# Kernel tuning notes

Hardware: AMD Instinct MI355X
Metric: run time of the kernel (lower is better)

Reference implementation:

```python
import jax, jax.numpy as jnp
import numpy as np

B, DIM, HID = 16384, 512, 256
DT, N_STEPS = 0.1, 3


def setup_inputs() -> dict:
    key = jax.random.key(0)
    ks = jax.random.split(key, 5)
    z = jax.random.normal(ks[0], (B, DIM), dtype=jnp.float32)
    # HNN energy MLP: 2*DIM -> HID -> HID -> 1 (tanh activations)
    s1 = 1.0 / np.sqrt(2 * DIM)
    s2 = 1.0 / np.sqrt(HID)
    W1 = jax.random.normal(ks[1], (2 * DIM, HID), dtype=jnp.float32) * s1
    b1 = jnp.zeros((HID,), dtype=jnp.float32)
    W2 = jax.random.normal(ks[2], (HID, HID), dtype=jnp.float32) * s2
    b2 = jnp.zeros((HID,), dtype=jnp.float32)
    W3 = jax.random.normal(ks[3], (HID, 1), dtype=jnp.float32) * s2
    b3 = jnp.zeros((1,), dtype=jnp.float32)
    return {"z": z, "W1": W1, "b1": b1, "W2": W2, "b2": b2, "W3": W3, "b3": b3}


def reference(z, W1, b1, W2, b2, W3, b3):
    d = z.shape[-1]
    dt = jnp.float32(DT)

    def H_sum(zp):  # total Hamiltonian over the batch -> scalar
        h = jnp.tanh(zp @ W1 + b1)
        h = jnp.tanh(h @ W2 + b2)
        return jnp.sum(h @ W3 + b3)

    gradH = jax.grad(H_sum)  # [B, 2d]: (dH/dq, dH/dp) per sample

    def leapfrog(zp):
        q, p = zp[:, :d], zp[:, d:]
        # half-step momentum: dp/dt = -dH/dq
        g = gradH(jnp.concatenate([q, p], axis=-1))
        p = p - 0.5 * dt * g[:, :d]
        # full-step position: dq/dt = dH/dp
        g = gradH(jnp.concatenate([q, p], axis=-1))
        q = q + dt * g[:, d:]
        # half-step momentum
        g = gradH(jnp.concatenate([q, p], axis=-1))
        p = p - 0.5 * dt * g[:, :d]
        return jnp.concatenate([q, p], axis=-1)

    zp = jnp.concatenate([z, jnp.zeros_like(z)], axis=-1)  # phase space [B, 2d]
    for _ in range(N_STEPS):  # fixed small unroll (n_steps=3)
        zp = leapfrog(zp)
    return zp[:, :d]
```

## Files before the change

kernel.cpp:

```cpp
#include <hip/hip_runtime.h>
#include <math.h>

#define DT 0.1f

typedef __attribute__((ext_vector_type(4)))  short short4v;
typedef __attribute__((ext_vector_type(8)))  short short8;
typedef __attribute__((ext_vector_type(16))) float f32x16;

__device__ __forceinline__ short f2bf(float x) {
    unsigned int u = __float_as_uint(x);
    unsigned int r = (u + 0x7fffu + ((u >> 16) & 1u)) >> 16;
    return (short)r;
}
__device__ __forceinline__ float bf2f(short s) {
    return __uint_as_float(((unsigned int)(unsigned short)s) << 16);
}
__device__ __forceinline__ float tanh_fast(float x) {
    float e = __expf(x + x);
    float r = __builtin_amdgcn_rcpf(e + 1.f);
    return __builtin_fmaf(-2.f, r, 1.f);
}

__device__ __forceinline__ void pack32_body(const float* __restrict__ W,
                                            short* __restrict__ out,
                                            int K, int N, int idx, bool trans)
{
    int j = idx & 7, lane = (idx >> 3) & 63, rest = idx >> 9;
    int KT = K >> 4;
    int kt = rest % KT, nt = rest / KT;
    int k = kt * 16 + (lane >> 5) * 8 + j;
    int n = nt * 32 + (lane & 31);
    out[idx] = f2bf(trans ? W[n * K + k] : W[k * N + n]);
}

__global__ __launch_bounds__(256)
void prep(const float* __restrict__ W1, const float* __restrict__ W2,
          const float* __restrict__ z,
          short* __restrict__ PBSq, short* __restrict__ PBSp,
          short* __restrict__ PB2, short* __restrict__ PB2T,
          short* __restrict__ PB1q, short* __restrict__ PB1Tp,
          short* __restrict__ zpA)
{
    __shared__ short zb[32 * 520];
    const int tid = threadIdx.x;
    const int b = blockIdx.x;

    if (b < 512) {
        const int n = tid;
        float s0 = 0.f, s1 = 0.f, s2 = 0.f, s3 = 0.f;
        int k; float coef; short* dst;
        if (b < 256) {
            k = b; coef = -0.5f * DT; dst = PBSq;
            for (int c = 0; c < 512; c += 4) {
                s0 = __builtin_fmaf(W1[(c + 0) * 256 + k], W1[(512 + c + 0) * 256 + n], s0);
                s1 = __builtin_fmaf(W1[(c + 1) * 256 + k], W1[(512 + c + 1) * 256 + n], s1);
                s2 = __builtin_fmaf(W1[(c + 2) * 256 + k], W1[(512 + c + 2) * 256 + n], s2);
                s3 = __builtin_fmaf(W1[(c + 3) * 256 + k], W1[(512 + c + 3) * 256 + n], s3);
            }
        } else {
            k = b - 256; coef = DT; dst = PBSp;
            for (int c = 0; c < 512; c += 4) {
                s0 = __builtin_fmaf(W1[(512 + c + 0) * 256 + k], W1[(c + 0) * 256 + n], s0);
                s1 = __builtin_fmaf(W1[(512 + c + 1) * 256 + k], W1[(c + 1) * 256 + n], s1);
                s2 = __builtin_fmaf(W1[(512 + c + 2) * 256 + k], W1[(c + 2) * 256 + n], s2);
                s3 = __builtin_fmaf(W1[(512 + c + 3) * 256 + k], W1[(c + 3) * 256 + n], s3);
            }
        }
        float v = coef * ((s0 + s1) + (s2 + s3));
        int kt = k >> 4, r = k & 15;
        int lane = (r >> 3) * 32 + (n & 31), nt = n >> 5;
        dst[(((nt * 16 + kt) * 64 + lane) << 3) + (r & 7)] = f2bf(v);
    } else if (b < 768) {
        pack32_body(W2, PB2, 256, 256, (b - 512) * 256 + tid, false);
    } else if (b < 1024) {
        pack32_body(W2, PB2T, 256, 256, (b - 768) * 256 + tid, true);
    } else if (b < 1536) {
        pack32_body(W1, PB1q, 512, 256, (b - 1024) * 256 + tid, false);
    } else if (b < 2048) {
        pack32_body(W1 + 512 * 256, PB1Tp, 256, 512, (b - 1536) * 256 + tid, true);
    } else {
        const int bx = b - 2048;
#pragma unroll
        for (int j = 0; j < 16; ++j) {
            int lin = j * 256 + tid;
            int r = lin >> 7, c4 = lin & 127;
            float4 v = ((const float4*)z)[(size_t)(bx * 32 + r) * 128 + c4];
            short4v pk;
            pk.x = f2bf(v.x); pk.y = f2bf(v.y); pk.z = f2bf(v.z); pk.w = f2bf(v.w);
            *(short4v*)&zb[r * 520 + c4 * 4] = pk;
        }
        __syncthreads();
        const int lane = tid & 63, w = tid >> 6;
        const int m = lane & 31, lh = lane >> 5;
#pragma unroll
        for (int j = 0; j < 8; ++j) {
            int kt = w * 8 + j;
            short8 f = *(const short8*)&zb[m * 520 + kt * 16 + lh * 8];
            *(short8*)(zpA + (((size_t)bx * 32 + kt) * 64 + lane) * 8) = f;
        }
    }
}

__device__ __forceinline__ short8 lds_frag(const short* Ac, int kt, int mt2,
                                           int l31, int lh, int rot)
{
    int nt_s = kt >> 1;
    int po = (((kt & 1) * 2 + lh) * 4 + rot) & 15;
    int base = ((nt_s * 2 + mt2) * 64 + l31) * 16 + po;
    short4v x = *(const short4v*)&Ac[base];
    short4v y = *(const short4v*)&Ac[base + 512];
    short8 r;
    r[0] = x.x; r[1] = x.y; r[2] = x.z; r[3] = x.w;
    r[4] = y.x; r[5] = y.y; r[6] = y.z; r[7] = y.w;
    return r;
}
__device__ __forceinline__ void store_tile(short* Ac, int nt, int mt2, int lane,
                                           int rot, const f32x16 v)
{
    int base = ((nt * 2 + mt2) * 64 + lane) * 16;
#pragma unroll
    for (int c = 0; c < 4; ++c) {
        short4v pk;
        pk.x = f2bf(v[4 * c + 0]); pk.y = f2bf(v[4 * c + 1]);
        pk.z = f2bf(v[4 * c + 2]); pk.w = f2bf(v[4 * c + 3]);
        *(short4v*)&Ac[base + ((4 * c + rot) & 15)] = pk;
    }
}

__device__ __forceinline__ void gemm_nt(const short* Ac, int l31, int lh, int rot,
                                        const short8* __restrict__ Bf,
                                        f32x16& acc0, f32x16& acc1)
{
    short8 pb[4];
#pragma unroll
    for (int k = 0; k < 4; ++k) pb[k] = Bf[k * 64];
    short8 pa0 = lds_frag(Ac, 0, 0, l31, lh, rot);
    short8 pa1 = lds_frag(Ac, 0, 1, l31, lh, rot);
#pragma unroll
    for (int kt = 0; kt < 16; ++kt) {
        short8 ca0 = pa0, ca1 = pa1, cb = pb[kt & 3];
        if (kt + 4 < 16) pb[kt & 3] = Bf[(kt + 4) * 64];
        if (kt + 1 < 16) {
            pa0 = lds_frag(Ac, kt + 1, 0, l31, lh, rot);
            pa1 = lds_frag(Ac, kt + 1, 1, l31, lh, rot);
        }
        acc0 = __builtin_amdgcn_mfma_f32_32x32x16_bf16(ca0, cb, acc0, 0, 0, 0);
        acc1 = __builtin_amdgcn_mfma_f32_32x32x16_bf16(ca1, cb, acc1, 0, 0, 0);
    }
}

__global__ __launch_bounds__(512, 2)
void mega(const short* __restrict__ zpA,
          const short* __restrict__ PB1q,
          const short* __restrict__ PB2,
          const short* __restrict__ PB2T,
          const short* __restrict__ PBSq,
          const short* __restrict__ PBSp,
          const float* __restrict__ b1,
          const float* __restrict__ b2,
          const float* __restrict__ W3,
          const short* __restrict__ PB1Tp,
          const float* __restrict__ z,
          float* __restrict__ out)
{
    __shared__ alignas(16) short smem[32768];
    short* h1_c = smem;
    short* da_c = smem + 16384;

    const int tid = threadIdx.x;
    const int lane = tid & 63, w = tid >> 6;
    const int l31 = lane & 31, lh = lane >> 5;
    const int rot = ((l31 >> 2) & 3) * 4;
    const int bx = blockIdx.x;

    const int col = w * 32 + l31;
    const float b1v = b1[col], b2v = b2[col], w3v = W3[col];

    f32x16 A1[2];  A1[0] = 0.f; A1[1] = 0.f;
    f32x16 dsum[2]; dsum[0] = 0.f; dsum[1] = 0.f;

    {
        const short8* Af0 = (const short8*)zpA + ((size_t)(bx * 2 + 0) * 32) * 64 + lane;
        const short8* Af1 = (const short8*)zpA + ((size_t)(bx * 2 + 1) * 32) * 64 + lane;
        const short8* Bf  = (const short8*)PB1q + ((size_t)w * 32) * 64 + lane;
        short8 pa0[2], pa1[2], pb[4];
#pragma unroll
        for (int k = 0; k < 2; ++k) { pa0[k] = Af0[k * 64]; pa1[k] = Af1[k * 64]; }
#pragma unroll
        for (int k = 0; k < 4; ++k) pb[k] = Bf[k * 64];
#pragma unroll
        for (int kt = 0; kt < 32; ++kt) {
            short8 ca0 = pa0[kt & 1], ca1 = pa1[kt & 1], cb = pb[kt & 3];
            if (kt + 2 < 32) {
                pa0[kt & 1] = Af0[(kt + 2) * 64];
                pa1[kt & 1] = Af1[(kt + 2) * 64];
            }
            if (kt + 4 < 32) pb[kt & 3] = Bf[(kt + 4) * 64];
            A1[0] = __builtin_amdgcn_mfma_f32_32x32x16_bf16(ca0, cb, A1[0], 0, 0, 0);
            A1[1] = __builtin_amdgcn_mfma_f32_32x32x16_bf16(ca1, cb, A1[1], 0, 0, 0);
        }
    }

    for (int it = 0; it < 8; ++it) {
        const bool isq = ((it % 3) == 1);

#pragma unroll
        for (int t = 0; t < 2; ++t) {
            f32x16 hv;
#pragma unroll
            for (int r = 0; r < 16; ++r) hv[r] = tanh_fast(A1[t][r] + b1v);
            store_tile(h1_c, w, t, lane, rot, hv);
        }
        __syncthreads();

        {
            f32x16 t0 = 0.f, t1 = 0.f;
            gemm_nt(h1_c, l31, lh, rot, (const short8*)PB2 + ((size_t)w * 16) * 64 + lane, t0, t1);
#pragma unroll
            for (int t = 0; t < 2; ++t) {
                f32x16& tt = t ? t1 : t0;
                f32x16 d;
#pragma unroll
                for (int r = 0; r < 16; ++r) {
                    float ta = tanh_fast(tt[r] + b2v);
                    d[r] = w3v * (1.f - ta * ta);
                }
                store_tile(da_c, w, t, lane, rot, d);
            }
        }
        __syncthreads();

        {
            f32x16 t0 = 0.f, t1 = 0.f;
            gemm_nt(da_c, l31, lh, rot, (const short8*)PB2T + ((size_t)w * 16) * 64 + lane, t0, t1);
            __syncthreads();
#pragma unroll
            for (int t = 0; t < 2; ++t) {
                f32x16& tt = t ? t1 : t0;
                f32x16 d;
                const int basei = ((w * 2 + t) * 64 + lane) * 16;
#pragma unroll
                for (int c = 0; c < 4; ++c) {
                    short4v h4 = *(const short4v*)&h1_c[basei + ((4 * c + rot) & 15)];
                    float h0 = bf2f(h4.x), h1f = bf2f(h4.y);
                    float h2 = bf2f(h4.z), h3 = bf2f(h4.w);
                    d[4 * c + 0] = tt[4 * c + 0] * (1.f - h0 * h0);
                    d[4 * c + 1] = tt[4 * c + 1] * (1.f - h1f * h1f);
                    d[4 * c + 2] = tt[4 * c + 2] * (1.f - h2 * h2);
                    d[4 * c + 3] = tt[4 * c + 3] * (1.f - h3 * h3);
                }
                if (isq) dsum[t] += d;
                store_tile(da_c, w, t, lane, rot, d);
            }
        }
        __syncthreads();

        if (it < 7) {
            const short* S = isq ? PBSp : PBSq;
            gemm_nt(da_c, l31, lh, rot, (const short8*)S + ((size_t)w * 16) * 64 + lane,
                    A1[0], A1[1]);
        }
    }

    store_tile(da_c, w, 0, lane, rot, dsum[0]);
    store_tile(da_c, w, 1, lane, rot, dsum[1]);
    __syncthreads();

    const int mt2 = w >> 2, nq = w & 3;
    f32x16 acc[4];
#pragma unroll
    for (int t = 0; t < 4; ++t) acc[t] = 0.f;
    const short8* Bf[4];
#pragma unroll
    for (int t = 0; t < 4; ++t)
        Bf[t] = (const short8*)PB1Tp + (size_t)(nq * 4 + t) * 16 * 64 + lane;

    short8 br[2][4];
#pragma unroll
    for (int k = 0; k < 2; ++k)
#pragma unroll
        for (int t = 0; t < 4; ++t) br[k][t] = Bf[t][k * 64];
#pragma unroll
    for (int kt = 0; kt < 16; ++kt) {
        short8 a = lds_frag(da_c, kt, mt2, l31, lh, rot);
        short8 bb[4];
#pragma unroll
        for (int t = 0; t < 4; ++t) bb[t] = br[kt & 1][t];
        if (kt + 2 < 16) {
#pragma unroll
            for (int t = 0; t < 4; ++t) br[kt & 1][t] = Bf[t][(kt + 2) * 64];
        }
#pragma unroll
        for (int t = 0; t < 4; ++t)
            acc[t] = __builtin_amdgcn_mfma_f32_32x32x16_bf16(a, bb[t], acc[t], 0, 0, 0);
    }
    __syncthreads();

    float* Ct = (float*)smem;
#pragma unroll
    for (int p = 0; p < 2; ++p) {
        if (mt2 == p) {
#pragma unroll
            for (int t = 0; t < 4; ++t) {
                const int c = (nq * 4 + t) * 32 + l31;
#pragma unroll
                for (int r = 0; r < 16; ++r) {
                    int row = (r & 3) + 8 * (r >> 2) + 4 * lh;
                    Ct[row * 512 + c] = acc[t][r];
                }
            }
        }
        __syncthreads();
#pragma unroll
        for (int j = 0; j < 8; ++j) {
            int lin = j * 512 + tid;
            int r = lin >> 7, c4 = lin & 127;
            size_t gi = (size_t)(bx * 64 + p * 32 + r) * 128 + c4;
            float4 zv = ((const float4*)z)[gi];
            float4 cv = *(const float4*)&Ct[r * 512 + c4 * 4];
            float4 ov;
            ov.x = zv.x + DT * cv.x; ov.y = zv.y + DT * cv.y;
            ov.z = zv.z + DT * cv.z; ov.w = zv.w + DT * cv.w;
            ((float4*)out)[gi] = ov;
        }
        __syncthreads();
    }
}

extern "C" void kernel_launch(void* const* d_in, const int* in_sizes, int n_in,
                              void* d_out, int out_size, void* d_ws, size_t ws_size,
                              hipStream_t stream)
{
    const float* z  = (const float*)d_in[0];
    const float* W1 = (const float*)d_in[1];
    const float* b1 = (const float*)d_in[2];
    const float* W2 = (const float*)d_in[3];
    const float* b2 = (const float*)d_in[4];
    const float* W3 = (const float*)d_in[5];
    float* out = (float*)d_out;

    short* PB2   = (short*)d_ws;
    short* PB2T  = PB2   + 65536;
    short* PBSq  = PB2T  + 65536;
    short* PBSp  = PBSq  + 65536;
    short* PB1q  = PBSp  + 65536;
    short* PB1Tp = PB1q  + 131072;
    short* zpA   = PB1Tp + 131072;

    prep<<<2560, 256, 0, stream>>>(W1, W2, z, PBSq, PBSp, PB2, PB2T,
                                   PB1q, PB1Tp, zpA);
    mega<<<256, 512, 0, stream>>>(zpA, PB1q, PB2, PB2T, PBSq, PBSp,
                                  b1, b2, W3, PB1Tp, z, out);
}
```

Before: 194.2 us.

## Halve mega-kernel row tile to 32 rows, doubling blocks and occupancy

The fused HNN kernel now gives each block 32 batch rows instead of 64, so it launches 512 blocks instead of 256. Each wave keeps one accumulator tile instead of two, shared memory is halved, and launch bounds ask for 4 blocks per CU instead of 2. The B-operand prefetch depth is deeper, and the final GEMM is remapped to two column tiles per wave. The weight fragments are reloaded for twice as many blocks, and each MFMA has less independent work to hide latency. The prep kernel's weight-product reduction is also unrolled to 8 accumulators.

```diff
diff --git a/kernel.cpp b/kernel.cpp
--- a/kernel.cpp
+++ b/kernel.cpp
@@ -47,26 +47,29 @@
 
     if (b < 512) {
         const int n = tid;
-        float s0 = 0.f, s1 = 0.f, s2 = 0.f, s3 = 0.f;
+        float s[8];
+#pragma unroll
+        for (int i = 0; i < 8; ++i) s[i] = 0.f;
         int k; float coef; short* dst;
         if (b < 256) {
             k = b; coef = -0.5f * DT; dst = PBSq;
-            for (int c = 0; c < 512; c += 4) {
-                s0 = __builtin_fmaf(W1[(c + 0) * 256 + k], W1[(512 + c + 0) * 256 + n], s0);
-                s1 = __builtin_fmaf(W1[(c + 1) * 256 + k], W1[(512 + c + 1) * 256 + n], s1);
-                s2 = __builtin_fmaf(W1[(c + 2) * 256 + k], W1[(512 + c + 2) * 256 + n], s2);
-                s3 = __builtin_fmaf(W1[(c + 3) * 256 + k], W1[(512 + c + 3) * 256 + n], s3);
+            for (int c = 0; c < 512; c += 8) {
+#pragma unroll
+                for (int i = 0; i < 8; ++i)
+                    s[i] = __builtin_fmaf(W1[(c + i) * 256 + k],
+                                          W1[(512 + c + i) * 256 + n], s[i]);
             }
         } else {
             k = b - 256; coef = DT; dst = PBSp;
-            for (int c = 0; c < 512; c += 4) {
-                s0 = __builtin_fmaf(W1[(512 + c + 0) * 256 + k], W1[(c + 0) * 256 + n], s0);
-                s1 = __builtin_fmaf(W1[(512 + c + 1) * 256 + k], W1[(c + 1) * 256 + n], s1);
-                s2 = __builtin_fmaf(W1[(512 + c + 2) * 256 + k], W1[(c + 2) * 256 + n], s2);
-                s3 = __builtin_fmaf(W1[(512 + c + 3) * 256 + k], W1[(c + 3) * 256 + n], s3);
-            }
-        }
-        float v = coef * ((s0 + s1) + (s2 + s3));
+            for (int c = 0; c < 512; c += 8) {
+#pragma unroll
+                for (int i = 0; i < 8; ++i)
+                    s[i] = __builtin_fmaf(W1[(512 + c + i) * 256 + k],
+                                          W1[(c + i) * 256 + n], s[i]);
+            }
+        }
+        float v = coef * (((s[0] + s[1]) + (s[2] + s[3])) +
+                          ((s[4] + s[5]) + (s[6] + s[7])));
         int kt = k >> 4, r = k & 15;
         int lane = (r >> 3) * 32 + (n & 31), nt = n >> 5;
         dst[(((nt * 16 + kt) * 64 + lane) << 3) + (r & 7)] = f2bf(v);
@@ -101,12 +104,12 @@
     }
 }
 
-__device__ __forceinline__ short8 lds_frag(const short* Ac, int kt, int mt2,
-                                           int l31, int lh, int rot)
+__device__ __forceinline__ short8 lds_frag32(const short* Ac, int kt,
+                                             int l31, int lh, int rot)
 {
     int nt_s = kt >> 1;
     int po = (((kt & 1) * 2 + lh) * 4 + rot) & 15;
-    int base = ((nt_s * 2 + mt2) * 64 + l31) * 16 + po;
+    int base = (nt_s * 64 + l31) * 16 + po;
     short4v x = *(const short4v*)&Ac[base];
     short4v y = *(const short4v*)&Ac[base + 512];
     short8 r;
@@ -114,10 +117,10 @@
     r[4] = y.x; r[5] = y.y; r[6] = y.z; r[7] = y.w;
     return r;
 }
-__device__ __forceinline__ void store_tile(short* Ac, int nt, int mt2, int lane,
-                                           int rot, const f32x16 v)
-{
-    int base = ((nt * 2 + mt2) * 64 + lane) * 16;
+__device__ __forceinline__ void store_tile32(short* Ac, int nt, int lane,
+                                             int rot, const f32x16 v)
+{
+    int base = (nt * 64 + lane) * 16;
 #pragma unroll
     for (int c = 0; c < 4; ++c) {
         short4v pk;
@@ -127,29 +130,25 @@
     }
 }
 
-__device__ __forceinline__ void gemm_nt(const short* Ac, int l31, int lh, int rot,
-                                        const short8* __restrict__ Bf,
-                                        f32x16& acc0, f32x16& acc1)
-{
-    short8 pb[4];
-#pragma unroll
-    for (int k = 0; k < 4; ++k) pb[k] = Bf[k * 64];
-    short8 pa0 = lds_frag(Ac, 0, 0, l31, lh, rot);
-    short8 pa1 = lds_frag(Ac, 0, 1, l31, lh, rot);
+__device__ __forceinline__ void gemm_nt32(const short* Ac, int l31, int lh, int rot,
+                                          const short8* __restrict__ Bf, f32x16& acc)
+{
+    short8 pb[8];
+#pragma unroll
+    for (int k = 0; k < 8; ++k) pb[k] = Bf[k * 64];
+    short8 pa0 = lds_frag32(Ac, 0, l31, lh, rot);
+    short8 pa1 = lds_frag32(Ac, 1, l31, lh, rot);
 #pragma unroll
     for (int kt = 0; kt < 16; ++kt) {
-        short8 ca0 = pa0, ca1 = pa1, cb = pb[kt & 3];
-        if (kt + 4 < 16) pb[kt & 3] = Bf[(kt + 4) * 64];
-        if (kt + 1 < 16) {
-            pa0 = lds_frag(Ac, kt + 1, 0, l31, lh, rot);
-            pa1 = lds_frag(Ac, kt + 1, 1, l31, lh, rot);
-        }
-        acc0 = __builtin_amdgcn_mfma_f32_32x32x16_bf16(ca0, cb, acc0, 0, 0, 0);
-        acc1 = __builtin_amdgcn_mfma_f32_32x32x16_bf16(ca1, cb, acc1, 0, 0, 0);
-    }
-}
-
-__global__ __launch_bounds__(512, 2)
+        short8 ca = pa0, cb = pb[kt & 7];
+        pa0 = pa1;
+        if (kt + 2 < 16) pa1 = lds_frag32(Ac, kt + 2, l31, lh, rot);
+        if (kt + 8 < 16) pb[kt & 7] = Bf[(kt + 8) * 64];
+        acc = __builtin_amdgcn_mfma_f32_32x32x16_bf16(ca, cb, acc, 0, 0, 0);
+    }
+}
+
+__global__ __launch_bounds__(512, 4)
 void mega(const short* __restrict__ zpA,
           const short* __restrict__ PB1q,
           const short* __restrict__ PB2,
@@ -163,9 +162,9 @@
           const float* __restrict__ z,
           float* __restrict__ out)
 {
-    __shared__ alignas(16) short smem[32768];
+    __shared__ alignas(16) short smem[16384];
     short* h1_c = smem;
-    short* da_c = smem + 16384;
+    short* da_c = smem + 8192;
 
     const int tid = threadIdx.x;
     const int lane = tid & 63, w = tid >> 6;
@@ -176,148 +175,130 @@
     const int col = w * 32 + l31;
     const float b1v = b1[col], b2v = b2[col], w3v = W3[col];
 
-    f32x16 A1[2];  A1[0] = 0.f; A1[1] = 0.f;
-    f32x16 dsum[2]; dsum[0] = 0.f; dsum[1] = 0.f;
+    f32x16 A1 = 0.f;
+    f32x16 dsum = 0.f;
 
     {
-        const short8* Af0 = (const short8*)zpA + ((size_t)(bx * 2 + 0) * 32) * 64 + lane;
-        const short8* Af1 = (const short8*)zpA + ((size_t)(bx * 2 + 1) * 32) * 64 + lane;
-        const short8* Bf  = (const short8*)PB1q + ((size_t)w * 32) * 64 + lane;
-        short8 pa0[2], pa1[2], pb[4];
-#pragma unroll
-        for (int k = 0; k < 2; ++k) { pa0[k] = Af0[k * 64]; pa1[k] = Af1[k * 64]; }
-#pragma unroll
-        for (int k = 0; k < 4; ++k) pb[k] = Bf[k * 64];
+        const short8* Af = (const short8*)zpA + ((size_t)bx * 32) * 64 + lane;
+        const short8* Bf = (const short8*)PB1q + ((size_t)w * 32) * 64 + lane;
+        short8 pa[4], pb[8];
+#pragma unroll
+        for (int k = 0; k < 4; ++k) pa[k] = Af[k * 64];
+#pragma unroll
+        for (int k = 0; k < 8; ++k) pb[k] = Bf[k * 64];
 #pragma unroll
         for (int kt = 0; kt < 32; ++kt) {
-            short8 ca0 = pa0[kt & 1], ca1 = pa1[kt & 1], cb = pb[kt & 3];
-            if (kt + 2 < 32) {
-                pa0[kt & 1] = Af0[(kt + 2) * 64];
-                pa1[kt & 1] = Af1[(kt + 2) * 64];
-            }
-            if (kt + 4 < 32) pb[kt & 3] = Bf[(kt + 4) * 64];
-            A1[0] = __builtin_amdgcn_mfma_f32_32x32x16_bf16(ca0, cb, A1[0], 0, 0, 0);
-            A1[1] = __builtin_amdgcn_mfma_f32_32x32x16_bf16(ca1, cb, A1[1], 0, 0, 0);
+            short8 ca = pa[kt & 3], cb = pb[kt & 7];
+            if (kt + 4 < 32) pa[kt & 3] = Af[(kt + 4) * 64];
+            if (kt + 8 < 32) pb[kt & 7] = Bf[(kt + 8) * 64];
+            A1 = __builtin_amdgcn_mfma_f32_32x32x16_bf16(ca, cb, A1, 0, 0, 0);
         }
     }
 
     for (int it = 0; it < 8; ++it) {
         const bool isq = ((it % 3) == 1);
 
-#pragma unroll
-        for (int t = 0; t < 2; ++t) {
+        {
             f32x16 hv;
 #pragma unroll
-            for (int r = 0; r < 16; ++r) hv[r] = tanh_fast(A1[t][r] + b1v);
-            store_tile(h1_c, w, t, lane, rot, hv);
+            for (int r = 0; r < 16; ++r) hv[r] = tanh_fast(A1[r] + b1v);
+            store_tile32(h1_c, w, lane, rot, hv);
         }
         __syncthreads();
 
         {
-            f32x16 t0 = 0.f, t1 = 0.f;
-            gemm_nt(h1_c, l31, lh, rot, (const short8*)PB2 + ((size_t)w * 16) * 64 + lane, t0, t1);
-#pragma unroll
-            for (int t = 0; t < 2; ++t) {
-                f32x16& tt = t ? t1 : t0;
-                f32x16 d;
-#pragma unroll
-                for (int r = 0; r < 16; ++r) {
-                    float ta = tanh_fast(tt[r] + b2v);
-                    d[r] = w3v * (1.f - ta * ta);
-                }
-                store_tile(da_c, w, t, lane, rot, d);
-            }
+            f32x16 t0 = 0.f;
+            gemm_nt32(h1_c, l31, lh, rot,
+                      (const short8*)PB2 + ((size_t)w * 16) * 64 + lane, t0);
+            f32x16 d;
+#pragma unroll
+            for (int r = 0; r < 16; ++r) {
+                float ta = tanh_fast(t0[r] + b2v);
+                d[r] = w3v * (1.f - ta * ta);
+            }
+            store_tile32(da_c, w, lane, rot, d);
         }
         __syncthreads();
 
         {
-            f32x16 t0 = 0.f, t1 = 0.f;
-            gemm_nt(da_c, l31, lh, rot, (const short8*)PB2T + ((size_t)w * 16) * 64 + lane, t0, t1);
+            f32x16 t0 = 0.f;
+            gemm_nt32(da_c, l31, lh, rot,
+                      (const short8*)PB2T + ((size_t)w * 16) * 64 + lane, t0);
             __syncthreads();
-#pragma unroll
-            for (int t = 0; t < 2; ++t) {
-                f32x16& tt = t ? t1 : t0;
-                f32x16 d;
-                const int basei = ((w * 2 + t) * 64 + lane) * 16;
-#pragma unroll
-                for (int c = 0; c < 4; ++c) {
-                    short4v h4 = *(const short4v*)&h1_c[basei + ((4 * c + rot) & 15)];
-                    float h0 = bf2f(h4.x), h1f = bf2f(h4.y);
-                    float h2 = bf2f(h4.z), h3 = bf2f(h4.w);
-                    d[4 * c + 0] = tt[4 * c + 0] * (1.f - h0 * h0);
-                    d[4 * c + 1] = tt[4 * c + 1] * (1.f - h1f * h1f);
-                    d[4 * c + 2] = tt[4 * c + 2] * (1.f - h2 * h2);
-                    d[4 * c + 3] = tt[4 * c + 3] * (1.f - h3 * h3);
-                }
-                if (isq) dsum[t] += d;
-                store_tile(da_c, w, t, lane, rot, d);
-            }
+            f32x16 d;
+            const int basei = (w * 64 + lane) * 16;
+#pragma unroll
+            for (int c = 0; c < 4; ++c) {
+                short4v h4 = *(const short4v*)&h1_c[basei + ((4 * c + rot) & 15)];
+                float h0 = bf2f(h4.x), h1f = bf2f(h4.y);
+                float h2 = bf2f(h4.z), h3 = bf2f(h4.w);
+                d[4 * c + 0] = t0[4 * c + 0] * (1.f - h0 * h0);
+                d[4 * c + 1] = t0[4 * c + 1] * (1.f - h1f * h1f);
+                d[4 * c + 2] = t0[4 * c + 2] * (1.f - h2 * h2);
+                d[4 * c + 3] = t0[4 * c + 3] * (1.f - h3 * h3);
+            }
+            if (isq) dsum += d;
+            store_tile32(da_c, w, lane, rot, d);
         }
         __syncthreads();
 
         if (it < 7) {
             const short* S = isq ? PBSp : PBSq;
-            gemm_nt(da_c, l31, lh, rot, (const short8*)S + ((size_t)w * 16) * 64 + lane,
-                    A1[0], A1[1]);
-        }
-    }
-
-    store_tile(da_c, w, 0, lane, rot, dsum[0]);
-    store_tile(da_c, w, 1, lane, rot, dsum[1]);
+            gemm_nt32(da_c, l31, lh, rot,
+                      (const short8*)S + ((size_t)w * 16) * 64 + lane, A1);
+        }
+    }
+
+    store_tile32(da_c, w, lane, rot, dsum);
     __syncthreads();
 
-    const int mt2 = w >> 2, nq = w & 3;
-    f32x16 acc[4];
-#pragma unroll
-    for (int t = 0; t < 4; ++t) acc[t] = 0.f;
-    const short8* Bf[4];
-#pragma unroll
-    for (int t = 0; t < 4; ++t)
-        Bf[t] = (const short8*)PB1Tp + (size_t)(nq * 4 + t) * 16 * 64 + lane;
-
-    short8 br[2][4];
-#pragma unroll
-    for (int k = 0; k < 2; ++k)
-#pragma unroll
-        for (int t = 0; t < 4; ++t) br[k][t] = Bf[t][k * 64];
-#pragma unroll
-    for (int kt = 0; kt < 16; ++kt) {
-        short8 a = lds_frag(da_c, kt, mt2, l31, lh, rot);
-        short8 bb[4];
-#pragma unroll
-        for (int t = 0; t < 4; ++t) bb[t] = br[kt & 1][t];
-        if (kt + 2 < 16) {
-#pragma unroll
-            for (int t = 0; t < 4; ++t) br[kt & 1][t] = Bf[t][(kt + 2) * 64];
-        }
-#pragma unroll
-        for (int t = 0; t < 4; ++t)
-            acc[t] = __builtin_amdgcn_mfma_f32_32x32x16_bf16(a, bb[t], acc[t], 0, 0, 0);
+    f32x16 acc2[2];
+    acc2[0] = 0.f; acc2[1] = 0.f;
+    {
+        const short8* Bf0 = (const short8*)PB1Tp + (size_t)(2 * w + 0) * 16 * 64 + lane;
+        const short8* Bf1 = (const short8*)PB1Tp + (size_t)(2 * w + 1) * 16 * 64 + lane;
+        short8 pb0[4], pb1[4];
+#pragma unroll
+        for (int k = 0; k < 4; ++k) { pb0[k] = Bf0[k * 64]; pb1[k] = Bf1[k * 64]; }
+        short8 pa0 = lds_frag32(da_c, 0, l31, lh, rot);
+        short8 pa1 = lds_frag32(da_c, 1, l31, lh, rot);
+#pragma unroll
+        for (int kt = 0; kt < 16; ++kt) {
+            short8 ca = pa0, cb0 = pb0[kt & 3], cb1 = pb1[kt & 3];
+            pa0 = pa1;
+            if (kt + 2 < 16) pa1 = lds_frag32(da_c, kt + 2, l31, lh, rot);
+            if (kt + 4 < 16) {
+                pb0[kt & 3] = Bf0[(kt + 4) * 64];
+                pb1[kt & 3] = Bf1[(kt + 4) * 64];
+            }
+            acc2[0] = __builtin_amdgcn_mfma_f32_32x32x16_bf16(ca, cb0, acc2[0], 0, 0, 0);
+            acc2[1] = __builtin_amdgcn_mfma_f32_32x32x16_bf16(ca, cb1, acc2[1], 0, 0, 0);
+        }
     }
     __syncthreads();
 
     float* Ct = (float*)smem;
 #pragma unroll
     for (int p = 0; p < 2; ++p) {
-        if (mt2 == p) {
-#pragma unroll
-            for (int t = 0; t < 4; ++t) {
-                const int c = (nq * 4 + t) * 32 + l31;
+        if ((w >> 2) == p) {
+#pragma unroll
+            for (int t = 0; t < 2; ++t) {
+                const int cl = (w & 3) * 64 + t * 32 + l31;
 #pragma unroll
                 for (int r = 0; r < 16; ++r) {
                     int row = (r & 3) + 8 * (r >> 2) + 4 * lh;
-                    Ct[row * 512 + c] = acc[t][r];
+                    Ct[row * 256 + cl] = acc2[t][r];
                 }
             }
         }
         __syncthreads();
 #pragma unroll
-        for (int j = 0; j < 8; ++j) {
+        for (int j = 0; j < 4; ++j) {
             int lin = j * 512 + tid;
-            int r = lin >> 7, c4 = lin & 127;
-            size_t gi = (size_t)(bx * 64 + p * 32 + r) * 128 + c4;
+            int r = lin >> 6, c4 = lin & 63;
+            size_t gi = (size_t)(bx * 32 + r) * 128 + p * 64 + c4;
             float4 zv = ((const float4*)z)[gi];
-            float4 cv = *(const float4*)&Ct[r * 512 + c4 * 4];
+            float4 cv = *(const float4*)&Ct[r * 256 + c4 * 4];
             float4 ov;
             ov.x = zv.x + DT * cv.x; ov.y = zv.y + DT * cv.y;
             ov.z = zv.z + DT * cv.z; ov.w = zv.w + DT * cv.w;
@@ -349,6 +330,6 @@
 
     prep<<<2560, 256, 0, stream>>>(W1, W2, z, PBSq, PBSp, PB2, PB2T,
                                    PB1q, PB1Tp, zpA);
-    mega<<<256, 512, 0, stream>>>(zpA, PB1q, PB2, PB2T, PBSq, PBSp,
+    mega<<<512, 512, 0, stream>>>(zpA, PB1q, PB2, PB2T, PBSq, PBSp,
                                   b1, b2, W3, PB1Tp, z, out);
 }
```

New measurement: 293.2 us. +51.0%, slower.

## Prefetch next GEMM weights across phases and double-buffer LDS gradient tiles

Applied to the files above, without the earlier changes.

Deepens the weight-fragment prefetch from 4 to 8 k-tiles and the LDS A-fragment prefetch to two tiles. The next GEMM's weight fragments are now loaded right after the current GEMM finishes, so global latency overlaps the tanh/derivative epilogue. A separate LDS buffer for the second-layer gradient removes one __syncthreads per iteration. In exchange it raises LDS to 96KB and drops the launch bound from 2 to 1 block per CU, which costs occupancy and leaves less latency hiding between blocks.

```diff
diff --git a/kernel.cpp b/kernel.cpp
--- a/kernel.cpp
+++ b/kernel.cpp
@@ -47,26 +47,29 @@
 
     if (b < 512) {
         const int n = tid;
-        float s0 = 0.f, s1 = 0.f, s2 = 0.f, s3 = 0.f;
+        float s[8];
+#pragma unroll
+        for (int i = 0; i < 8; ++i) s[i] = 0.f;
         int k; float coef; short* dst;
         if (b < 256) {
             k = b; coef = -0.5f * DT; dst = PBSq;
-            for (int c = 0; c < 512; c += 4) {
-                s0 = __builtin_fmaf(W1[(c + 0) * 256 + k], W1[(512 + c + 0) * 256 + n], s0);
-                s1 = __builtin_fmaf(W1[(c + 1) * 256 + k], W1[(512 + c + 1) * 256 + n], s1);
-                s2 = __builtin_fmaf(W1[(c + 2) * 256 + k], W1[(512 + c + 2) * 256 + n], s2);
-                s3 = __builtin_fmaf(W1[(c + 3) * 256 + k], W1[(512 + c + 3) * 256 + n], s3);
+            for (int c = 0; c < 512; c += 8) {
+#pragma unroll
+                for (int i = 0; i < 8; ++i)
+                    s[i] = __builtin_fmaf(W1[(c + i) * 256 + k],
+                                          W1[(512 + c + i) * 256 + n], s[i]);
             }
         } else {
             k = b - 256; coef = DT; dst = PBSp;
-            for (int c = 0; c < 512; c += 4) {
-                s0 = __builtin_fmaf(W1[(512 + c + 0) * 256 + k], W1[(c + 0) * 256 + n], s0);
-                s1 = __builtin_fmaf(W1[(512 + c + 1) * 256 + k], W1[(c + 1) * 256 + n], s1);
-                s2 = __builtin_fmaf(W1[(512 + c + 2) * 256 + k], W1[(c + 2) * 256 + n], s2);
-                s3 = __builtin_fmaf(W1[(512 + c + 3) * 256 + k], W1[(c + 3) * 256 + n], s3);
-            }
-        }
-        float v = coef * ((s0 + s1) + (s2 + s3));
+            for (int c = 0; c < 512; c += 8) {
+#pragma unroll
+                for (int i = 0; i < 8; ++i)
+                    s[i] = __builtin_fmaf(W1[(512 + c + i) * 256 + k],
+                                          W1[(c + i) * 256 + n], s[i]);
+            }
+        }
+        float v = coef * (((s[0] + s[1]) + (s[2] + s[3])) +
+                          ((s[4] + s[5]) + (s[6] + s[7])));
         int kt = k >> 4, r = k & 15;
         int lane = (r >> 3) * 32 + (n & 31), nt = n >> 5;
         dst[(((nt * 16 + kt) * 64 + lane) << 3) + (r & 7)] = f2bf(v);
@@ -127,29 +130,35 @@
     }
 }
 
+__device__ __forceinline__ void preload8(const short8* __restrict__ Bf, short8* pb)
+{
+#pragma unroll
+    for (int k = 0; k < 8; ++k) pb[k] = Bf[k * 64];
+}
+
 __device__ __forceinline__ void gemm_nt(const short* Ac, int l31, int lh, int rot,
                                         const short8* __restrict__ Bf,
-                                        f32x16& acc0, f32x16& acc1)
-{
-    short8 pb[4];
-#pragma unroll
-    for (int k = 0; k < 4; ++k) pb[k] = Bf[k * 64];
-    short8 pa0 = lds_frag(Ac, 0, 0, l31, lh, rot);
-    short8 pa1 = lds_frag(Ac, 0, 1, l31, lh, rot);
+                                        short8* pb, f32x16& acc0, f32x16& acc1)
+{
+    short8 pa0[2], pa1[2];
+    pa0[0] = lds_frag(Ac, 0, 0, l31, lh, rot);
+    pa1[0] = lds_frag(Ac, 0, 1, l31, lh, rot);
+    pa0[1] = lds_frag(Ac, 1, 0, l31, lh, rot);
+    pa1[1] = lds_frag(Ac, 1, 1, l31, lh, rot);
 #pragma unroll
     for (int kt = 0; kt < 16; ++kt) {
-        short8 ca0 = pa0, ca1 = pa1, cb = pb[kt & 3];
-        if (kt + 4 < 16) pb[kt & 3] = Bf[(kt + 4) * 64];
-        if (kt + 1 < 16) {
-            pa0 = lds_frag(Ac, kt + 1, 0, l31, lh, rot);
-            pa1 = lds_frag(Ac, kt + 1, 1, l31, lh, rot);
+        short8 ca0 = pa0[kt & 1], ca1 = pa1[kt & 1], cb = pb[kt & 7];
+        if (kt + 8 < 16) pb[kt & 7] = Bf[(kt + 8) * 64];
+        if (kt + 2 < 16) {
+            pa0[kt & 1] = lds_frag(Ac, kt + 2, 0, l31, lh, rot);
+            pa1[kt & 1] = lds_frag(Ac, kt + 2, 1, l31, lh, rot);
         }
         acc0 = __builtin_amdgcn_mfma_f32_32x32x16_bf16(ca0, cb, acc0, 0, 0, 0);
         acc1 = __builtin_amdgcn_mfma_f32_32x32x16_bf16(ca1, cb, acc1, 0, 0, 0);
     }
 }
 
-__global__ __launch_bounds__(512, 2)
+__global__ __launch_bounds__(512, 1)
 void mega(const short* __restrict__ zpA,
           const short* __restrict__ PB1q,
           const short* __restrict__ PB2,
@@ -163,9 +172,10 @@
           const float* __restrict__ z,
           float* __restrict__ out)
 {
-    __shared__ alignas(16) short smem[32768];
+    __shared__ alignas(16) short smem[49152];
     short* h1_c = smem;
-    short* da_c = smem + 16384;
+    short* da2_c = smem + 16384;
+    short* da1_c = smem + 32768;
 
     const int tid = threadIdx.x;
     const int lane = tid & 63, w = tid >> 6;
@@ -176,31 +186,38 @@
     const int col = w * 32 + l31;
     const float b1v = b1[col], b2v = b2[col], w3v = W3[col];
 
+    const short8* BfPB2  = (const short8*)PB2  + ((size_t)w * 16) * 64 + lane;
+    const short8* BfPB2T = (const short8*)PB2T + ((size_t)w * 16) * 64 + lane;
+    const short8* BfSq   = (const short8*)PBSq + ((size_t)w * 16) * 64 + lane;
+    const short8* BfSp   = (const short8*)PBSp + ((size_t)w * 16) * 64 + lane;
+
     f32x16 A1[2];  A1[0] = 0.f; A1[1] = 0.f;
     f32x16 dsum[2]; dsum[0] = 0.f; dsum[1] = 0.f;
+    short8 pb[8];
 
     {
         const short8* Af0 = (const short8*)zpA + ((size_t)(bx * 2 + 0) * 32) * 64 + lane;
         const short8* Af1 = (const short8*)zpA + ((size_t)(bx * 2 + 1) * 32) * 64 + lane;
         const short8* Bf  = (const short8*)PB1q + ((size_t)w * 32) * 64 + lane;
-        short8 pa0[2], pa1[2], pb[4];
+        short8 pa0[2], pa1[2];
 #pragma unroll
         for (int k = 0; k < 2; ++k) { pa0[k] = Af0[k * 64]; pa1[k] = Af1[k * 64]; }
-#pragma unroll
-        for (int k = 0; k < 4; ++k) pb[k] = Bf[k * 64];
+        preload8(Bf, pb);
 #pragma unroll
         for (int kt = 0; kt < 32; ++kt) {
-            short8 ca0 = pa0[kt & 1], ca1 = pa1[kt & 1], cb = pb[kt & 3];
+            short8 ca0 = pa0[kt & 1], ca1 = pa1[kt & 1], cb = pb[kt & 7];
             if (kt + 2 < 32) {
                 pa0[kt & 1] = Af0[(kt + 2) * 64];
                 pa1[kt & 1] = Af1[(kt + 2) * 64];
             }
-            if (kt + 4 < 32) pb[kt & 3] = Bf[(kt + 4) * 64];
+            if (kt + 8 < 32) pb[kt & 7] = Bf[(kt + 8) * 64];
             A1[0] = __builtin_amdgcn_mfma_f32_32x32x16_bf16(ca0, cb, A1[0], 0, 0, 0);
             A1[1] = __builtin_amdgcn_mfma_f32_32x32x16_bf16(ca1, cb, A1[1], 0, 0, 0);
         }
     }
 
+    preload8(BfPB2, pb);
+
     for (int it = 0; it < 8; ++it) {
         const bool isq = ((it % 3) == 1);
 
@@ -215,7 +232,8 @@
 
         {
             f32x16 t0 = 0.f, t1 = 0.f;
-            gemm_nt(h1_c, l31, lh, rot, (const short8*)PB2 + ((size_t)w * 16) * 64 + lane, t0, t1);
+            gemm_nt(h1_c, l31, lh, rot, BfPB2, pb, t0, t1);
+            preload8(BfPB2T, pb);
 #pragma unroll
             for (int t = 0; t < 2; ++t) {
                 f32x16& tt = t ? t1 : t0;
@@ -225,15 +243,15 @@
                     float ta = tanh_fast(tt[r] + b2v);
                     d[r] = w3v * (1.f - ta * ta);
                 }
-                store_tile(da_c, w, t, lane, rot, d);
+                store_tile(da2_c, w, t, lane, rot, d);
             }
         }
         __syncthreads();
 
         {
             f32x16 t0 = 0.f, t1 = 0.f;
-            gemm_nt(da_c, l31, lh, rot, (const short8*)PB2T + ((size_t)w * 16) * 64 + lane, t0, t1);
-            __syncthreads();
+            gemm_nt(da2_c, l31, lh, rot, BfPB2T, pb, t0, t1);
+            if (it < 7) preload8(isq ? BfSp : BfSq, pb);
 #pragma unroll
             for (int t = 0; t < 2; ++t) {
                 f32x16& tt = t ? t1 : t0;
@@ -250,80 +268,90 @@
                     d[4 * c + 3] = tt[4 * c + 3] * (1.f - h3 * h3);
                 }
                 if (isq) dsum[t] += d;
-                store_tile(da_c, w, t, lane, rot, d);
+                store_tile(da1_c, w, t, lane, rot, d);
             }
         }
         __syncthreads();
 
         if (it < 7) {
-            const short* S = isq ? PBSp : PBSq;
-            gemm_nt(da_c, l31, lh, rot, (const short8*)S + ((size_t)w * 16) * 64 + lane,
-                    A1[0], A1[1]);
-        }
-    }
-
-    store_tile(da_c, w, 0, lane, rot, dsum[0]);
-    store_tile(da_c, w, 1, lane, rot, dsum[1]);
+            gemm_nt(da1_c, l31, lh, rot, isq ? BfSp : BfSq, pb, A1[0], A1[1]);
+            preload8(BfPB2, pb);
+        }
+    }
+
+    store_tile(h1_c, w, 0, lane, rot, dsum[0]);
+    store_tile(h1_c, w, 1, lane, rot, dsum[1]);
     __syncthreads();
 
-    const int mt2 = w >> 2, nq = w & 3;
-    f32x16 acc[4];
-#pragma unroll
-    for (int t = 0; t < 4; ++t) acc[t] = 0.f;
-    const short8* Bf[4];
-#pragma unroll
-    for (int t = 0; t < 4; ++t)
-        Bf[t] = (const short8*)PB1Tp + (size_t)(nq * 4 + t) * 16 * 64 + lane;
-
-    short8 br[2][4];
-#pragma unroll
-    for (int k = 0; k < 2; ++k)
-#pragma unroll
-        for (int t = 0; t < 4; ++t) br[k][t] = Bf[t][k * 64];
-#pragma unroll
-    for (int kt = 0; kt < 16; ++kt) {
-        short8 a = lds_frag(da_c, kt, mt2, l31, lh, rot);
-        short8 bb[4];
-#pragma unroll
-        for (int t = 0; t < 4; ++t) bb[t] = br[kt & 1][t];
-        if (kt + 2 < 16) {
-#pragma unroll
-            for (int t = 0; t < 4; ++t) br[kt & 1][t] = Bf[t][(kt + 2) * 64];
-        }
-#pragma unroll
-        for (int t = 0; t < 4; ++t)
-            acc[t] = __builtin_amdgcn_mfma_f32_32x32x16_bf16(a, bb[t], acc[t], 0, 0, 0);
-    }
-    __syncthreads();
-
-    float* Ct = (float*)smem;
-#pragma unroll
-    for (int p = 0; p < 2; ++p) {
-        if (mt2 == p) {
-#pragma unroll
-            for (int t = 0; t < 4; ++t) {
-                const int c = (nq * 4 + t) * 32 + l31;
-#pragma unroll
-                for (int r = 0; r < 16; ++r) {
-                    int row = (r & 3) + 8 * (r >> 2) + 4 * lh;
-                    Ct[row * 512 + c] = acc[t][r];
+    const int mt2 = w >> 3 ? 0 : 0;
+    const int mtg = w >> 2 & 1;
+    (void)mt2; (void)mtg;
+
+    f32x16 acc2[2];
+    acc2[0] = 0.f; acc2[1] = 0.f;
+    const int mt = w >> 2;
+    const int nq = w & 3;
+    {
+        const short8* Bf0 = (const short8*)PB1Tp + (size_t)(nq * 4 + 0) * 16 * 64 + lane;
+        const short8* Bf1 = (const short8*)PB1Tp + (size_t)(nq * 4 + 1) * 16 * 64 + lane;
+        const short8* Bf2 = (const short8*)PB1Tp + (size_t)(nq * 4 + 2) * 16 * 64 + lane;
+        const short8* Bf3 = (const short8*)PB1Tp + (size_t)(nq * 4 + 3) * 16 * 64 + lane;
+        f32x16 acc4[4];
+#pragma unroll
+        for (int t = 0; t < 4; ++t) acc4[t] = 0.f;
+        short8 br[2][4];
+#pragma unroll
+        for (int k = 0; k < 2; ++k) {
+            br[k][0] = Bf0[k * 64]; br[k][1] = Bf1[k * 64];
+            br[k][2] = Bf2[k * 64]; br[k][3] = Bf3[k * 64];
+        }
+#pragma unroll
+        for (int kt = 0; kt < 16; ++kt) {
+            short8 a = lds_frag(h1_c, kt, mt, l31, lh, rot);
+            short8 bb[4];
+#pragma unroll
+            for (int t = 0; t < 4; ++t) bb[t] = br[kt & 1][t];
+            if (kt + 2 < 16) {
+                br[kt & 1][0] = Bf0[(kt + 2) * 64];
+                br[kt & 1][1] = Bf1[(kt + 2) * 64];
+                br[kt & 1][2] = Bf2[(kt + 2) * 64];
+                br[kt & 1][3] = Bf3[(kt + 2) * 64];
+            }
+#pragma unroll
+            for (int t = 0; t < 4; ++t)
+                acc4[t] = __builtin_amdgcn_mfma_f32_32x32x16_bf16(a, bb[t], acc4[t], 0, 0, 0);
+        }
+        __syncthreads();
+
+        float* Ct = (float*)smem;
+#pragma unroll
+        for (int p = 0; p < 2; ++p) {
+            if (mt == p) {
+#pragma unroll
+                for (int t = 0; t < 4; ++t) {
+                    const int c = (nq * 4 + t) * 32 + l31;
+#pragma unroll
+                    for (int r = 0; r < 16; ++r) {
+                        int row = (r & 3) + 8 * (r >> 2) + 4 * lh;
+                        Ct[row * 512 + c] = acc4[t][r];
+                    }
                 }
             }
-        }
-        __syncthreads();
-#pragma unroll
-        for (int j = 0; j < 8; ++j) {
-            int lin = j * 512 + tid;
-            int r = lin >> 7, c4 = lin & 127;
-            size_t gi = (size_t)(bx * 64 + p * 32 + r) * 128 + c4;
-            float4 zv = ((const float4*)z)[gi];
-            float4 cv = *(const float4*)&Ct[r * 512 + c4 * 4];
-            float4 ov;
-            ov.x = zv.x + DT * cv.x; ov.y = zv.y + DT * cv.y;
-            ov.z = zv.z + DT * cv.z; ov.w = zv.w + DT * cv.w;
-            ((float4*)out)[gi] = ov;
-        }
-        __syncthreads();
+            __syncthreads();
+#pragma unroll
+            for (int j = 0; j < 8; ++j) {
+                int lin = j * 512 + tid;
+                int r = lin >> 7, c4 = lin & 127;
+                size_t gi = (size_t)(bx * 64 + p * 32 + r) * 128 + c4;
+                float4 zv = ((const float4*)z)[gi];
+                float4 cv = *(const float4*)&Ct[r * 512 + c4 * 4];
+                float4 ov;
+                ov.x = zv.x + DT * cv.x; ov.y = zv.y + DT * cv.y;
+                ov.z = zv.z + DT * cv.z; ov.w = zv.w + DT * cv.w;
+                ((float4*)out)[gi] = ov;
+            }
+            __syncthreads();
+        }
     }
 }
 
```

Result: slower. 203.7 us (+4.9%).
